# Optimization experiments

Hardware: AMD Instinct MI355X
Metric: run time of the kernel (lower is better)

## Reference

```python
import jax, jax.numpy as jnp
import numpy as np

C = 16                 # channels
N = 1048576            # number of latent vectors (points)
FILTERS = (1, 3, 3, 3, 1)
INIT_SCALE = 8.0
LIKELIHOOD_BOUND = 1e-9


def setup_inputs() -> dict:
    key = jax.random.key(0)
    ks = jax.random.split(key, 10)
    d = {
        "inputs": jax.random.normal(ks[0], (N, C), jnp.float32),
        "noise": jax.random.uniform(ks[1], (N, C), jnp.float32),  # shifted by -0.5 in reference
    }
    scale = INIT_SCALE ** (1.0 / 4.0)  # len(filters)+1 = 4 layers
    for i in range(4):
        fi, fo = FILTERS[i], FILTERS[i + 1]
        init_m = np.log(np.expm1(1.0 / scale / fo)).astype(np.float32)
        d[f"m{i}"] = jnp.full((C, fo, fi), init_m, dtype=jnp.float32)
        d[f"b{i}"] = jax.random.uniform(ks[2 + i], (C, fo, 1), jnp.float32, -0.5, 0.5)
        d[f"f{i}"] = jax.random.uniform(ks[6 + i], (C, fo, 1), jnp.float32, -0.1, 0.1)
    return d


def _logits_cumulative(x, ms, bs, fs):
    # x: [C, 1, N]; each layer: [C, fo, fi] @ [C, fi, N] -> [C, fo, N]
    logits = x
    for M, b, f in zip(ms, bs, fs):
        logits = jnp.einsum('cof,cfn->con', jax.nn.softplus(M), logits) + b
        logits = logits + jnp.tanh(f) * jnp.tanh(logits)
    return logits


def reference(inputs, noise, m0, b0, f0, m1, b1, f1, m2, b2, f2, m3, b3, f3):
    # quantize_mode='noise': additive uniform(-0.5, 0.5) noise
    outputs = inputs + (noise - 0.5)                 # [N, C]
    x = outputs.T[:, None, :]                        # [C, 1, N]
    ms = [m0, m1, m2, m3]; bs = [b0, b1, b2, b3]; fs = [f0, f1, f2, f3]
    lower = _logits_cumulative(x - 0.5, ms, bs, fs)  # [C, 1, N]
    upper = _logits_cumulative(x + 0.5, ms, bs, fs)  # [C, 1, N]
    sign = jax.lax.stop_gradient(-jnp.sign(lower + upper))
    likelihood = jnp.abs(jax.nn.sigmoid(sign * upper) - jax.nn.sigmoid(sign * lower))
    likelihood = likelihood.reshape(C, N).T          # [N, C]
    likelihood = jnp.maximum(likelihood, LIKELIHOOD_BOUND)  # Low_bound (fwd)
    return (outputs, likelihood)
```

## Files before the change

### kernel.cpp

```cpp
#include <hip/hip_runtime.h>
#include <math.h>

#define CH 16
#define NINT 256
#define NPTS (NINT + 1)
#define TAB_ELEMS (CH * NPTS)
#define ORIGIN 8.0f
#define INV_H 16.0f


__device__ __forceinline__ float softplus_ref(float x) { return log1pf(expf(x)); }

__device__ float eval_net_exact(float x,
                                const float* sp0, const float* bb0, const float* tt0,
                                const float* sp1, const float* bb1, const float* tt1,
                                const float* sp2, const float* bb2, const float* tt2,
                                const float* sp3, float bb3, float tt3)
{
    float v0, v1, v2;
    {
        float l0 = fmaf(sp0[0], x, bb0[0]); v0 = fmaf(tt0[0], tanhf(l0), l0);
        float l1 = fmaf(sp0[1], x, bb0[1]); v1 = fmaf(tt0[1], tanhf(l1), l1);
        float l2 = fmaf(sp0[2], x, bb0[2]); v2 = fmaf(tt0[2], tanhf(l2), l2);
    }
    float w0, w1, w2;
    {
        float l0 = fmaf(sp1[0], v0, fmaf(sp1[1], v1, fmaf(sp1[2], v2, bb1[0])));
        float l1 = fmaf(sp1[3], v0, fmaf(sp1[4], v1, fmaf(sp1[5], v2, bb1[1])));
        float l2 = fmaf(sp1[6], v0, fmaf(sp1[7], v1, fmaf(sp1[8], v2, bb1[2])));
        w0 = fmaf(tt1[0], tanhf(l0), l0);
        w1 = fmaf(tt1[1], tanhf(l1), l1);
        w2 = fmaf(tt1[2], tanhf(l2), l2);
    }
    {
        float l0 = fmaf(sp2[0], w0, fmaf(sp2[1], w1, fmaf(sp2[2], w2, bb2[0])));
        float l1 = fmaf(sp2[3], w0, fmaf(sp2[4], w1, fmaf(sp2[5], w2, bb2[1])));
        float l2 = fmaf(sp2[6], w0, fmaf(sp2[7], w1, fmaf(sp2[8], w2, bb2[2])));
        v0 = fmaf(tt2[0], tanhf(l0), l0);
        v1 = fmaf(tt2[1], tanhf(l1), l1);
        v2 = fmaf(tt2[2], tanhf(l2), l2);
    }
    float l = fmaf(sp3[0], v0, fmaf(sp3[1], v1, fmaf(sp3[2], v2, bb3)));
    return fmaf(tt3, tanhf(l), l);
}

__global__ __launch_bounds__(256) void eb_table_kernel(
    const float* __restrict__ m0, const float* __restrict__ b0, const float* __restrict__ f0,
    const float* __restrict__ m1, const float* __restrict__ b1, const float* __restrict__ f1,
    const float* __restrict__ m2, const float* __restrict__ b2, const float* __restrict__ f2,
    const float* __restrict__ m3, const float* __restrict__ b3, const float* __restrict__ f3,
    float* __restrict__ tab)
{
    int t = blockIdx.x * blockDim.x + threadIdx.x;
    if (t >= TAB_ELEMS) return;
    int c = t / NPTS;
    int k = t - c * NPTS;

    float sp0[3], bb0[3], tt0[3];
    float sp1[9], bb1[3], tt1[3];
    float sp2[9], bb2[3], tt2[3];
    float sp3[3];
#pragma unroll
    for (int j = 0; j < 3; j++) {
        sp0[j] = softplus_ref(m0[c * 3 + j]);
        bb0[j] = b0[c * 3 + j];
        tt0[j] = tanhf(f0[c * 3 + j]);
        bb1[j] = b1[c * 3 + j];
        tt1[j] = tanhf(f1[c * 3 + j]);
        bb2[j] = b2[c * 3 + j];
        tt2[j] = tanhf(f2[c * 3 + j]);
        sp3[j] = softplus_ref(m3[c * 3 + j]);
    }
#pragma unroll
    for (int j = 0; j < 9; j++) {
        sp1[j] = softplus_ref(m1[c * 9 + j]);
        sp2[j] = softplus_ref(m2[c * 9 + j]);
    }
    float bb3 = b3[c];
    float tt3 = tanhf(f3[c]);

    float o = -ORIGIN + (float)k * (1.0f / INV_H);
    float lo = eval_net_exact(o - 0.5f, sp0, bb0, tt0, sp1, bb1, tt1, sp2, bb2, tt2, sp3, bb3, tt3);
    float up = eval_net_exact(o + 0.5f, sp0, bb0, tt0, sp1, bb1, tt1, sp2, bb2, tt2, sp3, bb3, tt3);

    float sum = lo + up;
    float s = (sum > 0.0f) ? -1.0f : ((sum < 0.0f) ? 1.0f : 0.0f);
    float su = 1.0f / (1.0f + expf(-s * up));
    float sl = 1.0f / (1.0f + expf(-s * lo));
    tab[t] = fmaxf(fabsf(su - sl), 1e-9f);
}


__global__ __launch_bounds__(256) void eb_main_kernel(
    const float4* __restrict__ inp, const float4* __restrict__ nz,
    const float* __restrict__ tab, float4* __restrict__ out, int nvec)
{
    __shared__ float lds[TAB_ELEMS];
    for (int j = threadIdx.x; j < TAB_ELEMS; j += 256) lds[j] = tab[j];
    __syncthreads();

    const int gtid = blockIdx.x * 256 + threadIdx.x;
    const int stride = gridDim.x * 256;

    for (int v = gtid; v < nvec; v += stride) {
        float4 a = inp[v];
        float4 b = nz[v];
        const int c0 = (v & 3) * 4;

        float4 o, lik;

        {
            float oe = a.x + b.x - 0.5f;
            float t = fminf(fmaxf(fmaf(oe, INV_H, ORIGIN * INV_H), 0.0f), 255.999f);
            int i = (int)t;
            float fr = t - (float)i;
            const float* p = &lds[(c0 + 0) * NPTS + i];
            float v0 = p[0], v1 = p[1];
            o.x = oe; lik.x = fmaxf(fmaf(fr, v1 - v0, v0), 1e-9f);
        }
        {
            float oe = a.y + b.y - 0.5f;
            float t = fminf(fmaxf(fmaf(oe, INV_H, ORIGIN * INV_H), 0.0f), 255.999f);
            int i = (int)t;
            float fr = t - (float)i;
            const float* p = &lds[(c0 + 1) * NPTS + i];
            float v0 = p[0], v1 = p[1];
            o.y = oe; lik.y = fmaxf(fmaf(fr, v1 - v0, v0), 1e-9f);
        }
        {
            float oe = a.z + b.z - 0.5f;
            float t = fminf(fmaxf(fmaf(oe, INV_H, ORIGIN * INV_H), 0.0f), 255.999f);
            int i = (int)t;
            float fr = t - (float)i;
            const float* p = &lds[(c0 + 2) * NPTS + i];
            float v0 = p[0], v1 = p[1];
            o.z = oe; lik.z = fmaxf(fmaf(fr, v1 - v0, v0), 1e-9f);
        }
        {
            float oe = a.w + b.w - 0.5f;
            float t = fminf(fmaxf(fmaf(oe, INV_H, ORIGIN * INV_H), 0.0f), 255.999f);
            int i = (int)t;
            float fr = t - (float)i;
            const float* p = &lds[(c0 + 3) * NPTS + i];
            float v0 = p[0], v1 = p[1];
            o.w = oe; lik.w = fmaxf(fmaf(fr, v1 - v0, v0), 1e-9f);
        }

        out[v] = o;
        out[nvec + v] = lik;
    }
}


extern "C" void kernel_launch(void* const* d_in, const int* in_sizes, int n_in,
                              void* d_out, int out_size, void* d_ws, size_t ws_size,
                              hipStream_t stream) {
    const float* inp = (const float*)d_in[0];
    const float* nz  = (const float*)d_in[1];
    const float* m0 = (const float*)d_in[2];
    const float* b0 = (const float*)d_in[3];
    const float* f0 = (const float*)d_in[4];
    const float* m1 = (const float*)d_in[5];
    const float* b1 = (const float*)d_in[6];
    const float* f1 = (const float*)d_in[7];
    const float* m2 = (const float*)d_in[8];
    const float* b2 = (const float*)d_in[9];
    const float* f2 = (const float*)d_in[10];
    const float* m3 = (const float*)d_in[11];
    const float* b3 = (const float*)d_in[12];
    const float* f3 = (const float*)d_in[13];

    float* tab = (float*)d_ws;
    const int total = in_sizes[0];
    const int nvec = total >> 2;

    hipLaunchKernelGGL(eb_table_kernel, dim3((TAB_ELEMS + 255) / 256), dim3(256), 0, stream,
                       m0, b0, f0, m1, b1, f1, m2, b2, f2, m3, b3, f3, tab);

    hipLaunchKernelGGL(eb_main_kernel, dim3(2048), dim3(256), 0, stream,
                       (const float4*)inp, (const float4*)nz, tab, (float4*)d_out, nvec);
}
```

Measured before the change: 270.1 us.

## Batch global loads per thread and overlap them with LDS table fill

Each thread now issues all eight float4 input and noise loads up front, before the barrier that guards the shared-memory table fill. The loads overlap with the table copy and give more memory-level parallelism. The grid-stride loop with 2048 blocks is replaced by one block per 2048 vectors, so the launch grows to 2048 blocks here. Since 256 is a multiple of 4, the channel offset is fixed per thread, which lets the row bases be hoisted. The trade-off is higher register use for the buffered loads, and every block now reloads the whole table.

After: 272.3 us. No clear change (+0.8%).

```diff
diff --git a/kernel.cpp b/kernel.cpp
--- a/kernel.cpp
+++ b/kernel.cpp
@@ -7,6 +7,7 @@
 #define TAB_ELEMS (CH * NPTS)
 #define ORIGIN 8.0f
 #define INV_H 16.0f
+#define ITERS 8
 
 
 __device__ __forceinline__ float softplus_ref(float x) { return log1pf(expf(x)); }
@@ -91,61 +92,52 @@
 }
 
 
+__device__ __forceinline__ float lookup(const float* lds, int row_base, float oe) {
+    float t = fminf(fmaxf(fmaf(oe, INV_H, ORIGIN * INV_H), 0.0f), 255.999f);
+    int i = (int)t;
+    float fr = t - (float)i;
+    const float* p = &lds[row_base + i];
+    float v0 = p[0], v1 = p[1];
+    return fmaxf(fmaf(fr, v1 - v0, v0), 1e-9f);
+}
+
 __global__ __launch_bounds__(256) void eb_main_kernel(
     const float4* __restrict__ inp, const float4* __restrict__ nz,
     const float* __restrict__ tab, float4* __restrict__ out, int nvec)
 {
     __shared__ float lds[TAB_ELEMS];
     for (int j = threadIdx.x; j < TAB_ELEMS; j += 256) lds[j] = tab[j];
+
+    const int tid = threadIdx.x;
+    const int blockStart = blockIdx.x * (256 * ITERS);
+    const int c0 = (tid & 3) * 4;
+    const int r0 = (c0 + 0) * NPTS;
+    const int r1 = (c0 + 1) * NPTS;
+    const int r2 = (c0 + 2) * NPTS;
+    const int r3 = (c0 + 3) * NPTS;
+
+    float4 a[ITERS], b[ITERS];
+#pragma unroll
+    for (int k = 0; k < ITERS; k++) {
+        int v = blockStart + k * 256 + tid;
+        if (v < nvec) { a[k] = inp[v]; b[k] = nz[v]; }
+    }
+
     __syncthreads();
 
-    const int gtid = blockIdx.x * 256 + threadIdx.x;
-    const int stride = gridDim.x * 256;
-
-    for (int v = gtid; v < nvec; v += stride) {
-        float4 a = inp[v];
-        float4 b = nz[v];
-        const int c0 = (v & 3) * 4;
-
+#pragma unroll
+    for (int k = 0; k < ITERS; k++) {
+        int v = blockStart + k * 256 + tid;
+        if (v >= nvec) break;
         float4 o, lik;
-
-        {
-            float oe = a.x + b.x - 0.5f;
-            float t = fminf(fmaxf(fmaf(oe, INV_H, ORIGIN * INV_H), 0.0f), 255.999f);
-            int i = (int)t;
-            float fr = t - (float)i;
-            const float* p = &lds[(c0 + 0) * NPTS + i];
-            float v0 = p[0], v1 = p[1];
-            o.x = oe; lik.x = fmaxf(fmaf(fr, v1 - v0, v0), 1e-9f);
-        }
-        {
-            float oe = a.y + b.y - 0.5f;
-            float t = fminf(fmaxf(fmaf(oe, INV_H, ORIGIN * INV_H), 0.0f), 255.999f);
-            int i = (int)t;
-            float fr = t - (float)i;
-            const float* p = &lds[(c0 + 1) * NPTS + i];
-            float v0 = p[0], v1 = p[1];
-            o.y = oe; lik.y = fmaxf(fmaf(fr, v1 - v0, v0), 1e-9f);
-        }
-        {
-            float oe = a.z + b.z - 0.5f;
-            float t = fminf(fmaxf(fmaf(oe, INV_H, ORIGIN * INV_H), 0.0f), 255.999f);
-            int i = (int)t;
-            float fr = t - (float)i;
-            const float* p = &lds[(c0 + 2) * NPTS + i];
-            float v0 = p[0], v1 = p[1];
-            o.z = oe; lik.z = fmaxf(fmaf(fr, v1 - v0, v0), 1e-9f);
-        }
-        {
-            float oe = a.w + b.w - 0.5f;
-            float t = fminf(fmaxf(fmaf(oe, INV_H, ORIGIN * INV_H), 0.0f), 255.999f);
-            int i = (int)t;
-            float fr = t - (float)i;
-            const float* p = &lds[(c0 + 3) * NPTS + i];
-            float v0 = p[0], v1 = p[1];
-            o.w = oe; lik.w = fmaxf(fmaf(fr, v1 - v0, v0), 1e-9f);
-        }
-
+        o.x = a[k].x + b[k].x - 0.5f;
+        o.y = a[k].y + b[k].y - 0.5f;
+        o.z = a[k].z + b[k].z - 0.5f;
+        o.w = a[k].w + b[k].w - 0.5f;
+        lik.x = lookup(lds, r0, o.x);
+        lik.y = lookup(lds, r1, o.y);
+        lik.z = lookup(lds, r2, o.z);
+        lik.w = lookup(lds, r3, o.w);
         out[v] = o;
         out[nvec + v] = lik;
     }
@@ -177,6 +169,8 @@
     hipLaunchKernelGGL(eb_table_kernel, dim3((TAB_ELEMS + 255) / 256), dim3(256), 0, stream,
                        m0, b0, f0, m1, b1, f1, m2, b2, f2, m3, b3, f3, tab);
 
-    hipLaunchKernelGGL(eb_main_kernel, dim3(2048), dim3(256), 0, stream,
+    const int chunk = 256 * ITERS;
+    const int blocks = (nvec + chunk - 1) / chunk;
+    hipLaunchKernelGGL(eb_main_kernel, dim3(blocks), dim3(256), 0, stream,
                        (const float4*)inp, (const float4*)nz, tab, (float4*)d_out, nvec);
 }
```
